# Kernel optimization log

Measured on AMD Instinct MI355X. Metric: run time of the kernel, lower is better.

The kernel has to match this reference:

```python
import jax, jax.numpy as jnp
import numpy as np
import math

C = 512
D = C // 4  # 128
SCALE = math.sqrt(D)

def setup_inputs() -> dict:
    key = jax.random.key(0)
    k1, k2, k3, k4 = jax.random.split(key, 4)
    x = jax.random.normal(k1, (8, C, 2048), dtype=jnp.float32)
    # q_conv and k_conv share the same weight (tied in the torch module)
    wqk = jax.random.normal(k2, (D, C), dtype=jnp.float32) * (1.0 / math.sqrt(C))
    wv = jax.random.normal(k3, (D, C), dtype=jnp.float32) * (1.0 / math.sqrt(C))
    bv = jax.random.normal(k4, (D,), dtype=jnp.float32) * 0.01
    return {"x": x, "wqk": wqk, "wv": wv, "bv": bv}

def reference(x, wqk, wv, bv):
    # x: [B, C, N]; 1x1 conv == matmul over channel dim
    xq = jnp.einsum('dc,bcn->bnd', wqk, x)          # [B, N, D]
    xk = jnp.einsum('dc,bcn->bdn', wqk, x)          # [B, D, N]
    xv = jnp.einsum('dc,bcn->bdn', wv, x) + bv[None, :, None]  # [B, D, N]
    energy = jnp.einsum('bnd,bdm->bnm', xq, xk) / SCALE  # [B, N, N]
    attention = jax.nn.softmax(energy, axis=-1)
    x_r = jnp.einsum('bdn,bnm->bdm', xv, attention)  # [B, D, N]
    return x_r
```

## Files before the change

kernel.cpp:

```cpp
#include <hip/hip_runtime.h>

typedef short short4v __attribute__((ext_vector_type(4)));
typedef short short8 __attribute__((ext_vector_type(8)));
typedef float floatx4 __attribute__((ext_vector_type(4)));
typedef unsigned int uint;
typedef unsigned short ushort;

#define CH 512
#define NN 2048
#define DD 128
#define RSCALE 0.08838834764831845f

__device__ __forceinline__ float bf2f(ushort u) {
    union { uint i; float f; } v; v.i = ((uint)u) << 16; return v.f;
}
__device__ __forceinline__ ushort f2bf(float f) {
    union { float f; uint u; } v; v.f = f;
    uint u = v.u;
    return (ushort)((u + 0x7fffu + ((u >> 16) & 1u)) >> 16);
}

__global__ __launch_bounds__(256) void k0_prep(
    const float* __restrict__ wqk, const float* __restrict__ wv,
    ushort* __restrict__ Wbf, float* __restrict__ lsum,
    float* __restrict__ out)
{
    int gid = blockIdx.x * 256 + threadIdx.x;
    float4 z; z.x = 0.f; z.y = 0.f; z.z = 0.f; z.w = 0.f;
    *(float4*)&out[gid * 4] = z;
    if (gid < 32768) {
        int base = gid * 4;
        const float* src = (base < 65536) ? (wqk + base) : (wv + base - 65536);
        float4 v = *(const float4*)src;
        short4v o;
        o[0] = (short)f2bf(v.x); o[1] = (short)f2bf(v.y);
        o[2] = (short)f2bf(v.z); o[3] = (short)f2bf(v.w);
        *(short4v*)&Wbf[base] = o;
    }
    if (gid < 16384) lsum[gid] = 0.0f;
}

__global__ __launch_bounds__(256) void k1_proj(
    const float* __restrict__ x,
    const ushort* __restrict__ Wbf,
    const float* __restrict__ bv,
    ushort* __restrict__ Q,
    ushort* __restrict__ VT)
{
    const int nt = blockIdx.x;
    const int b  = blockIdx.y;
    const int n0 = nt * 32;
    const int t = threadIdx.x;
    const int lane = t & 63, w = t >> 6, l15 = lane & 15, quad = lane >> 4;

    __shared__ __attribute__((aligned(16))) ushort As[32 * 40];
    __shared__ __attribute__((aligned(16))) ushort Bs[256 * 40];
    __shared__ __attribute__((aligned(16))) ushort Vt[128 * 40];

    floatx4 acc[2][4];
#pragma unroll
    for (int i = 0; i < 2; i++)
#pragma unroll
        for (int j = 0; j < 4; j++) acc[i][j] = (floatx4)(0.0f);

    const float* xb = x + b * (CH * NN) + n0;

    for (int c0 = 0; c0 < CH; c0 += 32) {
        {
            int n = t & 31, g = t >> 5;
            short4v v;
#pragma unroll
            for (int i = 0; i < 4; i++)
                v[i] = (short)f2bf(xb[(c0 + g * 4 + i) * NN + n]);
            *(short4v*)&As[n * 40 + g * 4] = v;
        }
#pragma unroll
        for (int rep = 0; rep < 4; rep++) {
            int idx = rep * 256 + t;
            int row = idx >> 2, g = idx & 3;
            *(short8*)&Bs[row * 40 + g * 8] = *(const short8*)&Wbf[row * CH + c0 + g * 8];
        }
        __syncthreads();
        short8 a0 = *(short8*)&As[(l15) * 40 + quad * 8];
        short8 a1 = *(short8*)&As[(16 + l15) * 40 + quad * 8];
#pragma unroll
        for (int dt2 = 0; dt2 < 4; dt2++) {
            short8 bf = *(short8*)&Bs[(w * 64 + dt2 * 16 + l15) * 40 + quad * 8];
            acc[0][dt2] = __builtin_amdgcn_mfma_f32_16x16x32_bf16(a0, bf, acc[0][dt2], 0, 0, 0);
            acc[1][dt2] = __builtin_amdgcn_mfma_f32_16x16x32_bf16(a1, bf, acc[1][dt2], 0, 0, 0);
        }
        __syncthreads();
    }

#pragma unroll
    for (int ns = 0; ns < 2; ns++)
#pragma unroll
        for (int dt2 = 0; dt2 < 4; dt2++) {
            int ds_ = w * 64 + dt2 * 16 + l15;
#pragma unroll
            for (int r = 0; r < 4; r++) {
                int nl = ns * 16 + quad * 4 + r;
                float val = acc[ns][dt2][r];
                if (ds_ < 128) {
                    Q[b * (NN * DD) + (n0 + nl) * DD + ds_] = f2bf(val);
                } else {
                    int dv = ds_ - 128;
                    Vt[dv * 40 + nl] = f2bf(val + bv[dv]);
                }
            }
        }
    __syncthreads();
#pragma unroll
    for (int rep = 0; rep < 2; rep++) {
        int idx = rep * 256 + t;
        int dv = idx >> 2, seg = idx & 3;
        *(short8*)&VT[((size_t)b * DD + dv) * NN + n0 + seg * 8] =
            *(short8*)&Vt[dv * 40 + seg * 8];
    }
}

__global__ __launch_bounds__(256) void kl_sum(
    const ushort* __restrict__ Q,
    float* __restrict__ lsum)
{
    int pid = blockIdx.x;
    const int b = blockIdx.y;
    int it = 0;
    while (pid >= (16 - it)) { pid -= (16 - it); it++; }
    const int jt = it + pid;
    const int i0 = it * 128, j0 = jt * 128;
    const int t = threadIdx.x;
    const int lane = t & 63, w = t >> 6, l15 = lane & 15, quad = lane >> 4;
    const int wi = (w >> 1) * 64, wj = (w & 1) * 64;

    __shared__ __attribute__((aligned(16))) ushort Qi[128 * 136];
    __shared__ __attribute__((aligned(16))) ushort Qj[128 * 136];

    const ushort* Qb = Q + b * (NN * DD);

#pragma unroll
    for (int rep = 0; rep < 8; rep++) {
        int idx = rep * 256 + t;
        int row = idx >> 4, g = idx & 15;
        *(short8*)&Qi[row * 136 + g * 8] = *(const short8*)&Qb[(i0 + row) * DD + g * 8];
        *(short8*)&Qj[row * 136 + g * 8] = *(const short8*)&Qb[(j0 + row) * DD + g * 8];
    }
    __syncthreads();

    floatx4 acc[4][4];
#pragma unroll
    for (int i = 0; i < 4; i++)
#pragma unroll
        for (int j = 0; j < 4; j++) acc[i][j] = (floatx4)(0.0f);

#pragma unroll
    for (int kd = 0; kd < 4; kd++) {
        short8 afr[4], bfr[4];
#pragma unroll
        for (int nt = 0; nt < 4; nt++)
            afr[nt] = *(short8*)&Qi[(wi + nt * 16 + l15) * 136 + kd * 32 + quad * 8];
#pragma unroll
        for (int mt = 0; mt < 4; mt++)
            bfr[mt] = *(short8*)&Qj[(wj + mt * 16 + l15) * 136 + kd * 32 + quad * 8];
#pragma unroll
        for (int nt = 0; nt < 4; nt++)
#pragma unroll
            for (int mt = 0; mt < 4; mt++)
                acc[nt][mt] = __builtin_amdgcn_mfma_f32_16x16x32_bf16(afr[nt], bfr[mt], acc[nt][mt], 0, 0, 0);
    }

    float cs[4] = {0.f, 0.f, 0.f, 0.f};
#pragma unroll
    for (int nt = 0; nt < 4; nt++) {
        float rs[4] = {0.f, 0.f, 0.f, 0.f};
#pragma unroll
        for (int mt = 0; mt < 4; mt++)
#pragma unroll
            for (int r = 0; r < 4; r++) {
                float p = __expf(acc[nt][mt][r] * RSCALE);
                rs[r] += p;
                cs[mt] += p;
            }
#pragma unroll
        for (int r = 0; r < 4; r++) {
            float s = rs[r];
            s += __shfl_xor(s, 1);
            s += __shfl_xor(s, 2);
            s += __shfl_xor(s, 4);
            s += __shfl_xor(s, 8);
            if (l15 == 0)
                atomicAdd(&lsum[b * NN + i0 + wi + nt * 16 + quad * 4 + r], s);
        }
    }
    if (it != jt) {
#pragma unroll
        for (int mt = 0; mt < 4; mt++) {
            float s = cs[mt];
            s += __shfl_xor(s, 16);
            s += __shfl_xor(s, 32);
            if (lane < 16)
                atomicAdd(&lsum[b * NN + j0 + wj + mt * 16 + l15], s);
        }
    }
}

__global__ __launch_bounds__(256) void k_fused(
    const ushort* __restrict__ Q,
    const ushort* __restrict__ VT,
    const float* __restrict__ lsum,
    float* __restrict__ out)
{
    const int mt = blockIdx.x;
    const int h  = blockIdx.y;
    const int b  = blockIdx.z;
    const int m0 = mt * 64;
    const int t = threadIdx.x;
    const int lane = t & 63, w = t >> 6, l15 = lane & 15, quad = lane >> 4;

    __shared__ __attribute__((aligned(16))) ushort Vs[128 * 72];
    __shared__ __attribute__((aligned(16))) ushort Ps[64 * 68];

    const ushort* Qb = Q + b * (NN * DD);
    const ushort* VTb = VT + (size_t)b * DD * NN;
    const float* lb = lsum + b * NN;

    short8 qm[4][4];
#pragma unroll
    for (int ms = 0; ms < 4; ms++)
#pragma unroll
        for (int kd = 0; kd < 4; kd++)
            qm[ms][kd] = *(const short8*)&Qb[(m0 + ms * 16 + l15) * DD + kd * 32 + quad * 8];

    floatx4 acc[2][4];
#pragma unroll
    for (int i = 0; i < 2; i++)
#pragma unroll
        for (int j = 0; j < 4; j++) acc[i][j] = (floatx4)(0.0f);

    const int nbeg = h * (NN / 4);
    for (int n0c = nbeg; n0c < nbeg + NN / 4; n0c += 64) {
        __syncthreads();

        short8 bq[4];
#pragma unroll
        for (int kd = 0; kd < 4; kd++)
            bq[kd] = *(const short8*)&Qb[(n0c + w * 16 + l15) * DD + kd * 32 + quad * 8];
        float lw = lb[n0c + w * 16 + l15];

        short8 vstage[4];
#pragma unroll
        for (int rep = 0; rep < 4; rep++) {
            int idx = rep * 256 + t;
            int d = idx >> 3, g = idx & 7;
            vstage[rep] = *(const short8*)&VTb[(size_t)d * NN + n0c + g * 8];
        }

        {
            float linv = 1.0f / lw;
#pragma unroll
            for (int ms = 0; ms < 4; ms++) {
                floatx4 s = (floatx4)(0.0f);
#pragma unroll
                for (int kd = 0; kd < 4; kd++)
                    s = __builtin_amdgcn_mfma_f32_16x16x32_bf16(qm[ms][kd], bq[kd], s, 0, 0, 0);
#pragma unroll
                for (int r = 0; r < 4; r++) {
                    float p = __expf(s[r] * RSCALE) * linv;
                    Ps[(ms * 16 + quad * 4 + r) * 68 + w * 16 + l15] = f2bf(p);
                }
            }
        }

#pragma unroll
        for (int rep = 0; rep < 4; rep++) {
            int idx = rep * 256 + t;
            int d = idx >> 3, g = idx & 7;
            *(short8*)&Vs[d * 72 + g * 8] = vstage[rep];
        }
        __syncthreads();

#pragma unroll
        for (int kn = 0; kn < 2; kn++) {
            short8 va0 = *(short8*)&Vs[(w * 32 + l15) * 72 + kn * 32 + quad * 8];
            short8 va1 = *(short8*)&Vs[(w * 32 + 16 + l15) * 72 + kn * 32 + quad * 8];
#pragma unroll
            for (int mf = 0; mf < 4; mf++) {
                short8 pb = *(short8*)&Ps[(mf * 16 + l15) * 68 + kn * 32 + quad * 8];
                acc[0][mf] = __builtin_amdgcn_mfma_f32_16x16x32_bf16(va0, pb, acc[0][mf], 0, 0, 0);
                acc[1][mf] = __builtin_amdgcn_mfma_f32_16x16x32_bf16(va1, pb, acc[1][mf], 0, 0, 0);
            }
        }
    }

    float* ob = out + (size_t)b * DD * NN;
#pragma unroll
    for (int dsub = 0; dsub < 2; dsub++)
#pragma unroll
        for (int mf = 0; mf < 4; mf++)
#pragma unroll
            for (int r = 0; r < 4; r++) {
                int d = w * 32 + dsub * 16 + quad * 4 + r;
                atomicAdd(&ob[(size_t)d * NN + m0 + mf * 16 + l15], acc[dsub][mf][r]);
            }
}

__global__ __launch_bounds__(256) void k1_fb(
    const float* __restrict__ x, const float* __restrict__ wqk,
    const float* __restrict__ wv, const float* __restrict__ bv,
    ushort* __restrict__ Q, ushort* __restrict__ V)
{
    const int nt = blockIdx.x;
    const int b  = blockIdx.y;
    const int n0 = nt * 32;
    const int t = threadIdx.x;
    const int lane = t & 63, w = t >> 6, l15 = lane & 15, quad = lane >> 4;

    __shared__ __attribute__((aligned(16))) ushort As[32 * 40];
    __shared__ __attribute__((aligned(16))) ushort Bs[256 * 40];

    floatx4 acc[2][4];
#pragma unroll
    for (int i = 0; i < 2; i++)
#pragma unroll
        for (int j = 0; j < 4; j++) acc[i][j] = (floatx4)(0.0f);

    const float* xb = x + b * (CH * NN) + n0;

    for (int c0 = 0; c0 < CH; c0 += 32) {
        {
            int n = t & 31, g = t >> 5;
            short4v v;
#pragma unroll
            for (int i = 0; i < 4; i++)
                v[i] = (short)f2bf(xb[(c0 + g * 4 + i) * NN + n]);
            *(short4v*)&As[n * 40 + g * 4] = v;
        }
#pragma unroll
        for (int rep = 0; rep < 16; rep++) {
            int idx = rep * 256 + t;
            int row = idx >> 4, cp = idx & 15;
            const float* wf = (row < 128) ? (wqk + row * CH) : (wv + (row - 128) * CH);
            uint pack = (uint)f2bf(wf[c0 + cp * 2]) | ((uint)f2bf(wf[c0 + cp * 2 + 1]) << 16);
            *(uint*)&Bs[row * 40 + cp * 2] = pack;
        }
        __syncthreads();
        short8 a0 = *(short8*)&As[(l15) * 40 + quad * 8];
        short8 a1 = *(short8*)&As[(16 + l15) * 40 + quad * 8];
#pragma unroll
        for (int dt2 = 0; dt2 < 4; dt2++) {
            short8 bf = *(short8*)&Bs[(w * 64 + dt2 * 16 + l15) * 40 + quad * 8];
            acc[0][dt2] = __builtin_amdgcn_mfma_f32_16x16x32_bf16(a0, bf, acc[0][dt2], 0, 0, 0);
            acc[1][dt2] = __builtin_amdgcn_mfma_f32_16x16x32_bf16(a1, bf, acc[1][dt2], 0, 0, 0);
        }
        __syncthreads();
    }
#pragma unroll
    for (int ns = 0; ns < 2; ns++)
#pragma unroll
        for (int dt2 = 0; dt2 < 4; dt2++) {
            int ds_ = w * 64 + dt2 * 16 + l15;
#pragma unroll
            for (int r = 0; r < 4; r++) {
                int n = n0 + ns * 16 + quad * 4 + r;
                float val = acc[ns][dt2][r];
                if (ds_ < 128) {
                    Q[b * (NN * DD) + n * DD + ds_] = f2bf(val);
                } else {
                    int dv = ds_ - 128;
                    V[b * (NN * DD) + n * DD + dv] = f2bf(val + bv[dv]);
                }
            }
        }
}

__global__ __launch_bounds__(256) void k2_norm(
    const ushort* __restrict__ Q, ushort* __restrict__ V)
{
    const int ntile = blockIdx.x;
    const int b = blockIdx.y;
    const int n0 = ntile * 64;
    const int t = threadIdx.x;
    const int lane = t & 63, w = t >> 6, l15 = lane & 15, quad = lane >> 4;

    __shared__ __attribute__((aligned(16))) ushort Qs[64 * 136];
    __shared__ __attribute__((aligned(16))) ushort Qm2[64 * 136];

    const ushort* Qb = Q + b * (NN * DD);

#pragma unroll
    for (int rep = 0; rep < 16; rep++) {
        int idx = rep * 256 + t;
        int row = idx >> 6, dp = idx & 63;
        *(uint*)&Qs[row * 136 + dp * 2] = *(const uint*)&Qb[(n0 + row) * DD + dp * 2];
    }
    __syncthreads();

    short8 afr[4];
#pragma unroll
    for (int kd = 0; kd < 4; kd++)
        afr[kd] = *(short8*)&Qs[(w * 16 + l15) * 136 + kd * 32 + quad * 8];

    float sums[4] = {0.f, 0.f, 0.f, 0.f};

    for (int m0 = 0; m0 < NN; m0 += 64) {
#pragma unroll
        for (int rep = 0; rep < 16; rep++) {
            int idx = rep * 256 + t;
            int row = idx >> 6, dp = idx & 63;
            *(uint*)&Qm2[row * 136 + dp * 2] = *(const uint*)&Qb[(m0 + row) * DD + dp * 2];
        }
        __syncthreads();
#pragma unroll
        for (int ct = 0; ct < 4; ct++) {
            floatx4 s = (floatx4)(0.0f);
#pragma unroll
            for (int kd = 0; kd < 4; kd++) {
                short8 bf = *(short8*)&Qm2[(ct * 16 + l15) * 136 + kd * 32 + quad * 8];
                s = __builtin_amdgcn_mfma_f32_16x16x32_bf16(afr[kd], bf, s, 0, 0, 0);
            }
#pragma unroll
            for (int r = 0; r < 4; r++)
                sums[r] += __expf(s[r] * RSCALE);
        }
        __syncthreads();
    }

#pragma unroll
    for (int r = 0; r < 4; r++) {
        float s = sums[r];
        s += __shfl_xor(s, 1);
        s += __shfl_xor(s, 2);
        s += __shfl_xor(s, 4);
        s += __shfl_xor(s, 8);
        sums[r] = s;
    }

    ushort* Vb = V + b * (NN * DD);
#pragma unroll
    for (int r = 0; r < 4; r++) {
        int n = n0 + w * 16 + quad * 4 + r;
        float inv = 1.0f / sums[r];
        short8 vv = *(short8*)&Vb[n * DD + l15 * 8];
        short8 o;
#pragma unroll
        for (int i = 0; i < 8; i++)
            o[i] = (short)f2bf(bf2f((ushort)vv[i]) * inv);
        *(short8*)&Vb[n * DD + l15 * 8] = o;
    }
}

__global__ __launch_bounds__(256) void k3_attn(
    const ushort* __restrict__ Q, const ushort* __restrict__ Vp,
    float* __restrict__ out)
{
    const int mtile = blockIdx.x;
    const int b = blockIdx.y;
    const int m0 = mtile * 64;
    const int t = threadIdx.x;
    const int lane = t & 63, w = t >> 6, l15 = lane & 15, quad = lane >> 4;

    __shared__ __attribute__((aligned(16))) ushort Qs[64 * 136];
    __shared__ __attribute__((aligned(16))) ushort Qn2[32 * 136];
    __shared__ __attribute__((aligned(16))) ushort Vs2[128 * 40];
    __shared__ __attribute__((aligned(16))) ushort Ps2[64 * 40];

    const ushort* Qb = Q + b * (NN * DD);
    const ushort* Vpb = Vp + b * (NN * DD);

#pragma unroll
    for (int rep = 0; rep < 16; rep++) {
        int idx = rep * 256 + t;
        int row = idx >> 6, dp = idx & 63;
        *(uint*)&Qs[row * 136 + dp * 2] = *(const uint*)&Qb[(m0 + row) * DD + dp * 2];
    }
    __syncthreads();

    short8 afr[4];
#pragma unroll
    for (int kd = 0; kd < 4; kd++)
        afr[kd] = *(short8*)&Qs[(w * 16 + l15) * 136 + kd * 32 + quad * 8];

    floatx4 acc[2][4];
#pragma unroll
    for (int s = 0; s < 2; s++)
#pragma unroll
        for (int mt = 0; mt < 4; mt++) acc[s][mt] = (floatx4)(0.0f);

    for (int n0c = 0; n0c < NN; n0c += 32) {
#pragma unroll
        for (int rep = 0; rep < 8; rep++) {
            int idx = rep * 256 + t;
            int row = idx >> 6, dp = idx & 63;
            *(uint*)&Qn2[row * 136 + dp * 2] = *(const uint*)&Qb[(n0c + row) * DD + dp * 2];
        }
#pragma unroll
        for (int rep = 0; rep < 8; rep++) {
            int idx = rep * 256 + t;
            int np = idx >> 7, d = idx & 127;
            uint v0 = Vpb[(n0c + np * 2) * DD + d];
            uint v1 = Vpb[(n0c + np * 2 + 1) * DD + d];
            *(uint*)&Vs2[d * 40 + np * 2] = v0 | (v1 << 16);
        }
        __syncthreads();

#pragma unroll
        for (int nt2 = 0; nt2 < 2; nt2++) {
            floatx4 s = (floatx4)(0.0f);
#pragma unroll
            for (int kd = 0; kd < 4; kd++) {
                short8 bf = *(short8*)&Qn2[(nt2 * 16 + l15) * 136 + kd * 32 + quad * 8];
                s = __builtin_amdgcn_mfma_f32_16x16x32_bf16(afr[kd], bf, s, 0, 0, 0);
            }
#pragma unroll
            for (int r = 0; r < 4; r++) {
                float p = __expf(s[r] * RSCALE);
                Ps2[(w * 16 + quad * 4 + r) * 40 + nt2 * 16 + l15] = f2bf(p);
            }
        }
        __syncthreads();

        short8 pb[4];
#pragma unroll
        for (int mt = 0; mt < 4; mt++)
            pb[mt] = *(short8*)&Ps2[(mt * 16 + l15) * 40 + quad * 8];
#pragma unroll
        for (int sub = 0; sub < 2; sub++) {
            short8 va = *(short8*)&Vs2[(w * 32 + sub * 16 + l15) * 40 + quad * 8];
#pragma unroll
            for (int mt = 0; mt < 4; mt++)
                acc[sub][mt] = __builtin_amdgcn_mfma_f32_16x16x32_bf16(va, pb[mt], acc[sub][mt], 0, 0, 0);
        }
        __syncthreads();
    }

    float* ob = out + (size_t)b * DD * NN;
#pragma unroll
    for (int sub = 0; sub < 2; sub++)
#pragma unroll
        for (int mt = 0; mt < 4; mt++)
#pragma unroll
            for (int r = 0; r < 4; r++) {
                int d = w * 32 + sub * 16 + quad * 4 + r;
                int m = m0 + mt * 16 + l15;
                ob[(size_t)d * NN + m] = acc[sub][mt][r];
            }
}

extern "C" void kernel_launch(void* const* d_in, const int* in_sizes, int n_in,
                              void* d_out, int out_size, void* d_ws, size_t ws_size,
                              hipStream_t stream) {
    const float* x   = (const float*)d_in[0];
    const float* wqk = (const float*)d_in[1];
    const float* wv  = (const float*)d_in[2];
    const float* bv  = (const float*)d_in[3];
    float* out = (float*)d_out;

    ushort* Q = (ushort*)d_ws;

    if (ws_size >= (size_t)16 * 1024 * 1024) {
        ushort* VT   = (ushort*)((char*)d_ws + (4u << 20));
        ushort* Wbf  = (ushort*)((char*)d_ws + (8u << 20));
        float*  lsum = (float*)((char*)d_ws + (8u << 20) + (256u << 10));

        k0_prep<<<2048, 256, 0, stream>>>(wqk, wv, Wbf, lsum, out);
        k1_proj<<<dim3(64, 8), 256, 0, stream>>>(x, Wbf, bv, Q, VT);
        kl_sum<<<dim3(136, 8), 256, 0, stream>>>(Q, lsum);
        k_fused<<<dim3(32, 4, 8), 256, 0, stream>>>(Q, VT, lsum, out);
    } else {
        ushort* V = (ushort*)((char*)d_ws + (4u << 20));
        k1_fb<<<dim3(64, 8), 256, 0, stream>>>(x, wqk, wv, bv, Q, V);
        k2_norm<<<dim3(32, 8), 256, 0, stream>>>(Q, V);
        k3_attn<<<dim3(32, 8), 256, 0, stream>>>(Q, V, out);
    }
}
```

Baseline: 174.8 us.

## Double-buffer Q and V tiles in LDS and halve the key-split in fused attention

The fused attention kernel now stages the key-side Q tile and the V tile into shared memory with double buffering, and prefetches the next chunk's global data into registers while the P·V MFMAs run. Query rows are also loaded through LDS with coalesced row-major reads. The key dimension is split two ways instead of four, so each block loops over twice as many chunks and issues half as many output atomics. In exchange, LDS use per block rises to about 78 KB, which may lower occupancy, and the grid shrinks to 512 blocks.

```diff
diff --git a/kernel.cpp b/kernel.cpp
--- a/kernel.cpp
+++ b/kernel.cpp
@@ -217,46 +217,71 @@
     const int t = threadIdx.x;
     const int lane = t & 63, w = t >> 6, l15 = lane & 15, quad = lane >> 4;
 
-    __shared__ __attribute__((aligned(16))) ushort Vs[128 * 72];
-    __shared__ __attribute__((aligned(16))) ushort Ps[64 * 68];
+    __shared__ __attribute__((aligned(16))) ushort sh[39168];
+    ushort* Qn0 = sh;
+    ushort* Qn1 = sh + 8704;
+    ushort* Vs0 = sh + 17408;
+    ushort* Vs1 = sh + 26112;
+    ushort* Ps  = sh + 34816;
 
     const ushort* Qb = Q + b * (NN * DD);
     const ushort* VTb = VT + (size_t)b * DD * NN;
     const float* lb = lsum + b * NN;
 
-    short8 qm[4][4];
-#pragma unroll
-    for (int ms = 0; ms < 4; ms++)
-#pragma unroll
-        for (int kd = 0; kd < 4; kd++)
-            qm[ms][kd] = *(const short8*)&Qb[(m0 + ms * 16 + l15) * DD + kd * 32 + quad * 8];
-
-    floatx4 acc[2][4];
-#pragma unroll
-    for (int i = 0; i < 2; i++)
-#pragma unroll
-        for (int j = 0; j < 4; j++) acc[i][j] = (floatx4)(0.0f);
-
-    const int nbeg = h * (NN / 4);
-    for (int n0c = nbeg; n0c < nbeg + NN / 4; n0c += 64) {
-        __syncthreads();
-
-        short8 bq[4];
-#pragma unroll
-        for (int kd = 0; kd < 4; kd++)
-            bq[kd] = *(const short8*)&Qb[(n0c + w * 16 + l15) * DD + kd * 32 + quad * 8];
-        float lw = lb[n0c + w * 16 + l15];
-
-        short8 vstage[4];
+    {
+        ushort* Qm = Vs0;
 #pragma unroll
         for (int rep = 0; rep < 4; rep++) {
             int idx = rep * 256 + t;
-            int d = idx >> 3, g = idx & 7;
-            vstage[rep] = *(const short8*)&VTb[(size_t)d * NN + n0c + g * 8];
-        }
+            int row = idx >> 4, g = idx & 15;
+            *(short8*)&Qm[row * 136 + g * 8] = *(const short8*)&Qb[(m0 + row) * DD + g * 8];
+        }
+    }
+    __syncthreads();
+    short8 qm[4][4];
+#pragma unroll
+    for (int ms = 0; ms < 4; ms++)
+#pragma unroll
+        for (int kd = 0; kd < 4; kd++)
+            qm[ms][kd] = *(short8*)&Vs0[(ms * 16 + l15) * 136 + kd * 32 + quad * 8];
+    __syncthreads();
+
+    const int nbeg = h * (NN / 2);
+#pragma unroll
+    for (int rep = 0; rep < 4; rep++) {
+        int idx = rep * 256 + t;
+        int row = idx >> 4, g = idx & 15;
+        *(short8*)&Qn0[row * 136 + g * 8] = *(const short8*)&Qb[(nbeg + row) * DD + g * 8];
+    }
+#pragma unroll
+    for (int rep = 0; rep < 4; rep++) {
+        int idx = rep * 256 + t;
+        int d = idx >> 3, g = idx & 7;
+        *(short8*)&Vs0[d * 68 + g * 8] = *(const short8*)&VTb[(size_t)d * NN + nbeg + g * 8];
+    }
+    float lw = lb[nbeg + w * 16 + l15];
+    __syncthreads();
+
+    floatx4 acc[2][4];
+#pragma unroll
+    for (int i = 0; i < 2; i++)
+#pragma unroll
+        for (int j = 0; j < 4; j++) acc[i][j] = (floatx4)(0.0f);
+
+    const int CCH = (NN / 2) / 64;
+    for (int i = 0; i < CCH; i++) {
+        const int n0c = nbeg + i * 64;
+        ushort* QnC = (i & 1) ? Qn1 : Qn0;
+        ushort* VsC = (i & 1) ? Vs1 : Vs0;
+        ushort* QnN = (i & 1) ? Qn0 : Qn1;
+        ushort* VsN = (i & 1) ? Vs0 : Vs1;
 
         {
             float linv = 1.0f / lw;
+            short8 bq[4];
+#pragma unroll
+            for (int kd = 0; kd < 4; kd++)
+                bq[kd] = *(short8*)&QnC[(w * 16 + l15) * 136 + kd * 32 + quad * 8];
 #pragma unroll
             for (int ms = 0; ms < 4; ms++) {
                 floatx4 s = (floatx4)(0.0f);
@@ -270,19 +295,31 @@
                 }
             }
         }
-
-#pragma unroll
-        for (int rep = 0; rep < 4; rep++) {
-            int idx = rep * 256 + t;
-            int d = idx >> 3, g = idx & 7;
-            *(short8*)&Vs[d * 72 + g * 8] = vstage[rep];
-        }
-        __syncthreads();
+        __syncthreads();
+
+        short8 qstage[4], vstage[4];
+        const bool more = (i + 1 < CCH);
+        if (more) {
+            const int n1 = n0c + 64;
+#pragma unroll
+            for (int rep = 0; rep < 4; rep++) {
+                int idx = rep * 256 + t;
+                int row = idx >> 4, g = idx & 15;
+                qstage[rep] = *(const short8*)&Qb[(n1 + row) * DD + g * 8];
+            }
+#pragma unroll
+            for (int rep = 0; rep < 4; rep++) {
+                int idx = rep * 256 + t;
+                int d = idx >> 3, g = idx & 7;
+                vstage[rep] = *(const short8*)&VTb[(size_t)d * NN + n1 + g * 8];
+            }
+            lw = lb[n1 + w * 16 + l15];
+        }
 
 #pragma unroll
         for (int kn = 0; kn < 2; kn++) {
-            short8 va0 = *(short8*)&Vs[(w * 32 + l15) * 72 + kn * 32 + quad * 8];
-            short8 va1 = *(short8*)&Vs[(w * 32 + 16 + l15) * 72 + kn * 32 + quad * 8];
+            short8 va0 = *(short8*)&VsC[(w * 32 + l15) * 68 + kn * 32 + quad * 8];
+            short8 va1 = *(short8*)&VsC[(w * 32 + 16 + l15) * 68 + kn * 32 + quad * 8];
 #pragma unroll
             for (int mf = 0; mf < 4; mf++) {
                 short8 pb = *(short8*)&Ps[(mf * 16 + l15) * 68 + kn * 32 + quad * 8];
@@ -290,6 +327,22 @@
                 acc[1][mf] = __builtin_amdgcn_mfma_f32_16x16x32_bf16(va1, pb, acc[1][mf], 0, 0, 0);
             }
         }
+
+        if (more) {
+#pragma unroll
+            for (int rep = 0; rep < 4; rep++) {
+                int idx = rep * 256 + t;
+                int row = idx >> 4, g = idx & 15;
+                *(short8*)&QnN[row * 136 + g * 8] = qstage[rep];
+            }
+#pragma unroll
+            for (int rep = 0; rep < 4; rep++) {
+                int idx = rep * 256 + t;
+                int d = idx >> 3, g = idx & 7;
+                *(short8*)&VsN[d * 68 + g * 8] = vstage[rep];
+            }
+        }
+        __syncthreads();
     }
 
     float* ob = out + (size_t)b * DD * NN;
@@ -565,7 +618,7 @@
         k0_prep<<<2048, 256, 0, stream>>>(wqk, wv, Wbf, lsum, out);
         k1_proj<<<dim3(64, 8), 256, 0, stream>>>(x, Wbf, bv, Q, VT);
         kl_sum<<<dim3(136, 8), 256, 0, stream>>>(Q, lsum);
-        k_fused<<<dim3(32, 4, 8), 256, 0, stream>>>(Q, VT, lsum, out);
+        k_fused<<<dim3(32, 2, 8), 256, 0, stream>>>(Q, VT, lsum, out);
     } else {
         ushort* V = (ushort*)((char*)d_ws + (4u << 20));
         k1_fb<<<dim3(64, 8), 256, 0, stream>>>(x, wqk, wv, bv, Q, V);
```

Result: slower. 188.7 us (+8.0%).
